# Performance work log

Measured on AMD Instinct MI355X. Metric: run time of the kernel, lower is better.

The kernel has to match this reference:

```python
import jax, jax.numpy as jnp
import numpy as np

L, H, D, DH, DFF = 6, 8, 512, 64, 2048
EPS = 1e-5


def setup_inputs() -> dict:
    key = jax.random.key(0)
    ks = jax.random.split(key, 20)
    B, S, T = 16, 512, 512
    s = 0.02
    inp = {
        "x": jax.random.normal(ks[0], (B, S, D), jnp.float32),
        "y": jax.random.normal(ks[1], (B, T, D), jnp.float32),
        # self-attention per-head projections, stacked over layers and heads
        "Wq1": jax.random.normal(ks[2], (L, H, D, DH), jnp.float32) * s,
        "Wk1": jax.random.normal(ks[3], (L, H, D, DH), jnp.float32) * s,
        "Wv1": jax.random.normal(ks[4], (L, H, D, DH), jnp.float32) * s,
        "Wo1": jax.random.normal(ks[5], (L, D, D), jnp.float32) * s,
        # cross-attention
        "Wq2": jax.random.normal(ks[6], (L, H, D, DH), jnp.float32) * s,
        "Wk2": jax.random.normal(ks[7], (L, H, D, DH), jnp.float32) * s,
        "Wv2": jax.random.normal(ks[8], (L, H, D, DH), jnp.float32) * s,
        "Wo2": jax.random.normal(ks[9], (L, D, D), jnp.float32) * s,
        # position-wise FFN
        "W1": jax.random.normal(ks[10], (L, D, DFF), jnp.float32) * s,
        "bf1": jnp.zeros((L, DFF), jnp.float32),
        "W2": jax.random.normal(ks[11], (L, DFF, D), jnp.float32) * s,
        "bf2": jnp.zeros((L, D), jnp.float32),
        # layer norms
        "ln1_g": jnp.ones((L, D), jnp.float32), "ln1_b": jnp.zeros((L, D), jnp.float32),
        "ln2_g": jnp.ones((L, D), jnp.float32), "ln2_b": jnp.zeros((L, D), jnp.float32),
        "ln3_g": jnp.ones((L, D), jnp.float32), "ln3_b": jnp.zeros((L, D), jnp.float32),
    }
    return inp


def _layer_norm(x, g, b):
    m = jnp.mean(x, axis=-1, keepdims=True)
    v = jnp.mean(jnp.square(x - m), axis=-1, keepdims=True)
    return (x - m) * jax.lax.rsqrt(v + EPS) * g + b


def _mha(q_in, kv_in, Wq, Wk, Wv, Wo, causal):
    # Wq/Wk/Wv: [H, D, DH]; batched equivalent of the per-head Linear loop
    q = jnp.einsum("bsd,hdk->bhsk", q_in, Wq)
    k = jnp.einsum("btd,hdk->bhtk", kv_in, Wk)
    v = jnp.einsum("btd,hdk->bhtk", kv_in, Wv)
    scores = jnp.einsum("bhsk,bhtk->bhst", q, k) / jnp.sqrt(jnp.float32(DH))
    if causal:
        S, T = scores.shape[-2], scores.shape[-1]
        mask = jnp.tril(jnp.ones((S, T), bool))
        scores = jnp.where(mask, scores, -jnp.inf)
    p = jax.nn.softmax(scores, axis=-1)
    out = jnp.einsum("bhst,bhtk->bhsk", p, v)
    B, _, S, _ = out.shape
    out = out.transpose(0, 2, 1, 3).reshape(B, S, H * DH)  # concat heads (dim=2 order)
    return out @ Wo


def reference(x, y, Wq1, Wk1, Wv1, Wo1, Wq2, Wk2, Wv2, Wo2,
              W1, bf1, W2, bf2, ln1_g, ln1_b, ln2_g, ln2_b, ln3_g, ln3_b):
    for l in range(L):
        # masked self-attention + residual + LN  (dropout = identity in eval)
        a1 = _mha(x, x, Wq1[l], Wk1[l], Wv1[l], Wo1[l], causal=True)
        h1 = _layer_norm(a1 + x, ln1_g[l], ln1_b[l])
        # cross-attention (queries from decoder, K/V from encoder output y)
        a2 = _mha(h1, y, Wq2[l], Wk2[l], Wv2[l], Wo2[l], causal=False)
        h2 = _layer_norm(a2 + h1, ln2_g[l], ln2_b[l])
        # position-wise FFN (batched over all positions)
        f = jax.nn.relu(h2 @ W1[l] + bf1[l]) @ W2[l] + bf2[l]
        x = _layer_norm(f + h2, ln3_g[l], ln3_b[l])
    return x
```

## Files before the change

kernel.cpp:

```cpp
#include <hip/hip_runtime.h>

typedef __bf16 bf16;
typedef __attribute__((ext_vector_type(8))) __bf16 bf16x8;
typedef __attribute__((ext_vector_type(4))) __bf16 bf16x4;
typedef __attribute__((ext_vector_type(4))) float f32x4;

#define GL16(gp, lp) __builtin_amdgcn_global_load_lds( \
    (const __attribute__((address_space(1))) unsigned int*)(gp), \
    (__attribute__((address_space(3))) unsigned int*)(lp), 16, 0, 0)

__device__ __forceinline__ f32x4 mfma16(bf16x8 a, bf16x8 b, f32x4 c) {
  return __builtin_amdgcn_mfma_f32_16x16x32_bf16(a, b, c, 0, 0, 0);
}

template<int BN, int RELU, int BIAS, int RES, int OUTB>
__global__ __launch_bounds__(256, 2) void gemm_k(
    const bf16* __restrict__ A, const bf16* __restrict__ Bt,
    float* __restrict__ Cf, bf16* __restrict__ Cb,
    const float* __restrict__ bias, const bf16* __restrict__ resid,
    int M, int N, int K)
{
  constexpr int MI = 4;
  constexpr int NI = BN / 32;
  __shared__ __align__(16) bf16 Al[3][128 * 32];
  __shared__ __align__(16) bf16 Bl[3][BN * 32];
  const int tid = threadIdx.x;
  const int wid = tid >> 6, lane = tid & 63;
  const int g = lane >> 4, l16 = lane & 15;

  int lin = blockIdx.x + gridDim.x * blockIdx.y;
  const int nwg = gridDim.x * gridDim.y;
  if ((nwg & 7) == 0) lin = (lin & 7) * (nwg >> 3) + (lin >> 3);
  const int bx = lin % gridDim.x, by = lin / gridDim.x;

  const int bm = by * 128, bn = bx * BN;
  const int wm = (wid >> 1) * 64;
  const int wn = (wid & 1) * (BN / 2);

  const f32x4 z4 = {0.f, 0.f, 0.f, 0.f};
  f32x4 acc[MI][NI];
#pragma unroll
  for (int i = 0; i < MI; ++i)
#pragma unroll
    for (int j = 0; j < NI; ++j) acc[i][j] = z4;

  const int srow = tid >> 2;
  const int scs = (((tid & 3) ^ ((srow >> 1) & 3)) * 8);
  const bf16* Ag = A + (size_t)(bm + srow) * K + scs;
  const bf16* Bg = Bt + (size_t)(bn + srow) * K + scs;
  const size_t half = (size_t)64 * K;

  auto stage = [&](int sel, int k0) {
    GL16(Ag + k0, &Al[sel][tid * 8]);
    GL16(Ag + k0 + half, &Al[sel][2048 + tid * 8]);
    GL16(Bg + k0, &Bl[sel][tid * 8]);
    if constexpr (BN == 128) GL16(Bg + k0 + half, &Bl[sel][2048 + tid * 8]);
  };
  constexpr int NL = 2 + BN / 64;

  const int nsteps = K >> 5;
  stage(0, 0);
  stage(1, 32);
  int cur = 0;
  for (int s = 0; s < nsteps; ++s) {
    __builtin_amdgcn_sched_barrier(0);
    if (s + 1 < nsteps) {
      if constexpr (NL == 4)
        asm volatile("s_waitcnt vmcnt(4)" ::: "memory");
      else
        asm volatile("s_waitcnt vmcnt(3)" ::: "memory");
    } else {
      asm volatile("s_waitcnt vmcnt(0)" ::: "memory");
    }
    __builtin_amdgcn_sched_barrier(0);
    __builtin_amdgcn_s_barrier();
    if (s + 2 < nsteps) {
      int pre = cur + 2; if (pre >= 3) pre -= 3;
      stage(pre, (s + 2) * 32);
    }
    bf16x8 af[MI], bfr[NI];
#pragma unroll
    for (int mi = 0; mi < MI; ++mi) {
      const int row = wm + mi * 16 + l16;
      af[mi] = *(const bf16x8*)&Al[cur][row * 32 + (g ^ ((row >> 1) & 3)) * 8];
    }
#pragma unroll
    for (int ni = 0; ni < NI; ++ni) {
      const int row = wn + ni * 16 + l16;
      bfr[ni] = *(const bf16x8*)&Bl[cur][row * 32 + (g ^ ((row >> 1) & 3)) * 8];
    }
#pragma unroll
    for (int mi = 0; mi < MI; ++mi)
#pragma unroll
      for (int ni = 0; ni < NI; ++ni)
        acc[mi][ni] = mfma16(af[mi], bfr[ni], acc[mi][ni]);
    ++cur; if (cur >= 3) cur = 0;
  }

#pragma unroll
  for (int mi = 0; mi < MI; ++mi) {
#pragma unroll
    for (int ni = 0; ni < NI; ++ni) {
#pragma unroll
      for (int r = 0; r < 4; ++r) {
        const int row = bm + wm + mi * 16 + g * 4 + r;
        const int col = bn + wn + ni * 16 + l16;
        float v = acc[mi][ni][r];
        if (BIAS) v += bias[col];
        const size_t idx = (size_t)row * N + col;
        if (RES)  v += (float)resid[idx];
        if (RELU) v = fmaxf(v, 0.f);
        if (OUTB) Cb[idx] = (bf16)v;
        else      Cf[idx] = v;
      }
    }
  }
}

template<int CAUSAL>
__global__ __launch_bounds__(256, 4) void attn_k(
    const bf16* __restrict__ Q, const bf16* __restrict__ Kg,
    const bf16* __restrict__ VT, bf16* __restrict__ O, int qs, int kvs)
{
  __shared__ __align__(16) bf16 Kl[2][64 * 64];
  __shared__ __align__(16) bf16 Vl[2][64 * 64];
  __shared__ __align__(16) bf16 plb[4 * 16 * 64];
  const int tid = threadIdx.x;
  const int wid = tid >> 6, lane = tid & 63;
  const int g = lane >> 4, l16 = lane & 15;

  int lin = blockIdx.x + 8 * blockIdx.y + 64 * blockIdx.z;
  lin = (lin & 7) * 128 + (lin >> 3);
  const int qt = lin & 7, h = (lin >> 3) & 7, b = lin >> 6;

  const int q0 = qt * 64 + wid * 16;
  const size_t tokQ = (size_t)b * 512 + q0;

  const bf16* qp = Q + (tokQ + l16) * (size_t)qs + h * 64 + g * 8;
  const bf16x8 qf0 = *(const bf16x8*)qp;
  const bf16x8 qf1 = *(const bf16x8*)(qp + 32);

  const int sr = tid >> 3;
  const int cs2 = ((((tid & 7) * 16) ^ ((sr & 7) << 4)) >> 1);
  const bf16* Ksrc = Kg + ((size_t)b * 512 + sr) * kvs + h * 64 + cs2;
  const bf16* Vsrc = VT + (size_t)(b * 8 + h) * 64 * 512 + (size_t)sr * 512 + cs2;
  bf16* pw = plb + wid * 1024;

  auto stage = [&](int sel, int t0) {
    GL16(Ksrc + (size_t)t0 * kvs, &Kl[sel][tid * 8]);
    GL16(Ksrc + (size_t)(t0 + 32) * kvs, &Kl[sel][tid * 8 + 2048]);
    GL16(Vsrc + t0, &Vl[sel][tid * 8]);
    GL16(Vsrc + 32 * 512 + t0, &Vl[sel][tid * 8 + 2048]);
  };

  const f32x4 z4 = {0.f, 0.f, 0.f, 0.f};
  float m[4], ls[4];
  f32x4 o[4];
#pragma unroll
  for (int r = 0; r < 4; ++r) { m[r] = -1e30f; ls[r] = 0.f; o[r] = z4; }

  const int sw = (l16 & 7) << 4;
  const int ktmax = CAUSAL ? qt : 7;
  stage(0, 0);
  int cur = 0;
  for (int kt = 0; kt <= ktmax; ++kt) {
    const int t0 = kt * 64;
    __builtin_amdgcn_sched_barrier(0);
    asm volatile("s_waitcnt vmcnt(0)" ::: "memory");
    __builtin_amdgcn_s_barrier();
    if (kt < ktmax) stage(cur ^ 1, t0 + 64);

    f32x4 sc[4];
#pragma unroll
    for (int jt = 0; jt < 4; ++jt) {
      const int rk = jt * 16 + l16;
      const bf16x8 kf0 = *(const bf16x8*)&Kl[cur][rk * 64 + (((g * 16) ^ sw) >> 1)];
      const bf16x8 kf1 = *(const bf16x8*)&Kl[cur][rk * 64 + (((g * 16 + 64) ^ sw) >> 1)];
      sc[jt] = mfma16(qf0, kf0, z4);
      sc[jt] = mfma16(qf1, kf1, sc[jt]);
    }
#pragma unroll
    for (int r = 0; r < 4; ++r) {
      const int q = g * 4 + r;
      const int srow = q0 + q;
      const int qs7 = (q & 7) << 4;
      float pv[4];
      float mx = -1e30f;
#pragma unroll
      for (int jt = 0; jt < 4; ++jt) {
        float v = sc[jt][r] * 0.125f;
        if (CAUSAL && (t0 + jt * 16 + l16) > srow) v = -1e30f;
        pv[jt] = v;
        mx = fmaxf(mx, v);
      }
#pragma unroll
      for (int msk = 8; msk; msk >>= 1) mx = fmaxf(mx, __shfl_xor(mx, msk));
      const float mn = fmaxf(m[r], mx);
      const float corr = __expf(m[r] - mn);
      float s = 0.f;
#pragma unroll
      for (int jt = 0; jt < 4; ++jt) {
        const float p = __expf(pv[jt] - mn);
        s += p;
        const int sb = (((jt * 16 + l16) * 2) ^ qs7) >> 1;
        pw[q * 64 + sb] = (bf16)p;
      }
#pragma unroll
      for (int msk = 8; msk; msk >>= 1) s += __shfl_xor(s, msk);
      ls[r] = ls[r] * corr + s;
      m[r] = mn;
#pragma unroll
      for (int j = 0; j < 4; ++j) o[j][r] *= corr;
    }
    asm volatile("s_waitcnt lgkmcnt(0)" ::: "memory");
    __builtin_amdgcn_sched_barrier(0);
    const bf16x8 pa0 = *(const bf16x8*)&pw[l16 * 64 + (((g * 16) ^ sw) >> 1)];
    const bf16x8 pa1 = *(const bf16x8*)&pw[l16 * 64 + (((g * 16 + 64) ^ sw) >> 1)];
#pragma unroll
    for (int j = 0; j < 4; ++j) {
      const int rv = j * 16 + l16;
      const bf16x8 vf0 = *(const bf16x8*)&Vl[cur][rv * 64 + (((g * 16) ^ sw) >> 1)];
      const bf16x8 vf1 = *(const bf16x8*)&Vl[cur][rv * 64 + (((g * 16 + 64) ^ sw) >> 1)];
      o[j] = mfma16(pa0, vf0, o[j]);
      o[j] = mfma16(pa1, vf1, o[j]);
    }
    cur ^= 1;
  }
#pragma unroll
  for (int r = 0; r < 4; ++r) {
    const float inv = 1.f / ls[r];
    bf16* op = O + (tokQ + g * 4 + r) * 512 + h * 64;
#pragma unroll
    for (int j = 0; j < 4; ++j) op[j * 16 + l16] = (bf16)(o[j][r] * inv);
  }
}

__global__ void vtrans(const bf16* __restrict__ src, bf16* __restrict__ dst,
                       int stride)
{
  __shared__ bf16 t[64][65];
  const int bh = blockIdx.z;
  const int b = bh >> 3, h = bh & 7;
  const int t0 = blockIdx.x * 64;
  const int tx = threadIdx.x, ty = threadIdx.y;
  src += ((size_t)b * 512 + t0) * stride + h * 64;
  dst += (size_t)bh * 64 * 512 + t0;
#pragma unroll
  for (int j = 0; j < 64; j += 4)
    t[ty + j][tx] = src[(size_t)(ty + j) * stride + tx];
  __syncthreads();
#pragma unroll
  for (int j = 0; j < 64; j += 4)
    dst[(size_t)(ty + j) * 512 + tx] = t[tx][ty + j];
}

__global__ __launch_bounds__(256) void ln_k(
    const float* __restrict__ z, const float* __restrict__ gam,
    const float* __restrict__ bet, float* __restrict__ of,
    bf16* __restrict__ ob)
{
  const int wid = threadIdx.x >> 6, lane = threadIdx.x & 63;
  const int row = blockIdx.x * 4 + wid;
  const f32x4* zr = (const f32x4*)(z + (size_t)row * 512);
  const f32x4 a = zr[lane], c = zr[lane + 64];
  float s = 0.f, ss = 0.f;
#pragma unroll
  for (int e = 0; e < 4; ++e) {
    s += a[e] + c[e];
    ss += a[e] * a[e] + c[e] * c[e];
  }
#pragma unroll
  for (int msk = 32; msk; msk >>= 1) {
    s += __shfl_xor(s, msk);
    ss += __shfl_xor(ss, msk);
  }
  const float mean = s * (1.f / 512.f);
  const float var = ss * (1.f / 512.f) - mean * mean;
  const float rstd = rsqrtf(var + 1e-5f);
  const f32x4* gp = (const f32x4*)gam;
  const f32x4* bp = (const f32x4*)bet;
  const f32x4 g0 = gp[lane], g1 = gp[lane + 64];
  const f32x4 b0 = bp[lane], b1 = bp[lane + 64];
  f32x4 o0, o1;
#pragma unroll
  for (int e = 0; e < 4; ++e) {
    o0[e] = (a[e] - mean) * rstd * g0[e] + b0[e];
    o1[e] = (c[e] - mean) * rstd * g1[e] + b1[e];
  }
  if (of) {
    f32x4* ofr = (f32x4*)(of + (size_t)row * 512);
    ofr[lane] = o0;
    ofr[lane + 64] = o1;
  }
  if (ob) {
    bf16x4 c0, c1;
#pragma unroll
    for (int e = 0; e < 4; ++e) { c0[e] = (bf16)o0[e]; c1[e] = (bf16)o1[e]; }
    bf16x4* obr = (bf16x4*)(ob + (size_t)row * 512);
    obr[lane] = c0;
    obr[lane + 64] = c1;
  }
}

__global__ void transpose_cast(const float* __restrict__ src, bf16* __restrict__ dst,
                               int R, int C, int bpl, size_t lstride, size_t boff)
{
  __shared__ float t[32][33];
  const int z = blockIdx.z;
  src += (size_t)z * R * C;
  dst += (size_t)(z / bpl) * lstride + (size_t)(z % bpl) * ((size_t)R * C) + boff;
  const int c0 = blockIdx.x * 32, r0 = blockIdx.y * 32;
  const int tx = threadIdx.x, ty = threadIdx.y;
#pragma unroll
  for (int j = 0; j < 32; j += 8)
    t[ty + j][tx] = src[(size_t)(r0 + ty + j) * C + c0 + tx];
  __syncthreads();
#pragma unroll
  for (int j = 0; j < 32; j += 8)
    dst[(size_t)(c0 + ty + j) * R + r0 + tx] = (bf16)t[tx][ty + j];
}

__global__ void cast4(const float* __restrict__ s, bf16* __restrict__ d)
{
  const int i = blockIdx.x * 256 + threadIdx.x;
  const f32x4 v = ((const f32x4*)s)[i];
  bf16x4 c;
#pragma unroll
  for (int e = 0; e < 4; ++e) c[e] = (bf16)v[e];
  ((bf16x4*)d)[i] = c;
}

extern "C" void kernel_launch(void* const* d_in, const int* in_sizes, int n_in,
                              void* d_out, int out_size, void* d_ws, size_t ws_size,
                              hipStream_t stream)
{
  (void)in_sizes; (void)n_in; (void)out_size; (void)ws_size;
  const float* x   = (const float*)d_in[0];
  const float* y   = (const float*)d_in[1];
  const float* Wq1 = (const float*)d_in[2];
  const float* Wk1 = (const float*)d_in[3];
  const float* Wv1 = (const float*)d_in[4];
  const float* Wo1 = (const float*)d_in[5];
  const float* Wq2 = (const float*)d_in[6];
  const float* Wk2 = (const float*)d_in[7];
  const float* Wv2 = (const float*)d_in[8];
  const float* Wo2 = (const float*)d_in[9];
  const float* W1  = (const float*)d_in[10];
  const float* b1  = (const float*)d_in[11];
  const float* W2  = (const float*)d_in[12];
  const float* b2  = (const float*)d_in[13];
  const float* ln1g = (const float*)d_in[14];
  const float* ln1b = (const float*)d_in[15];
  const float* ln2g = (const float*)d_in[16];
  const float* ln2b = (const float*)d_in[17];
  const float* ln3g = (const float*)d_in[18];
  const float* ln3b = (const float*)d_in[19];

  char* ws = (char*)d_ws;
  size_t off = 0;
  auto alloc = [&](size_t bytes) -> void* {
    void* p = (void*)(ws + off);
    off += (bytes + 255) & ~(size_t)255;
    return p;
  };

  bf16* wqkv1t = (bf16*)alloc((size_t)6 * 1536 * 512 * 2);
  bf16* wo1t   = (bf16*)alloc((size_t)6 * 512 * 512 * 2);
  bf16* wq2t   = (bf16*)alloc((size_t)6 * 512 * 512 * 2);
  bf16* wkv2t  = (bf16*)alloc((size_t)6 * 1024 * 512 * 2);
  bf16* wo2t   = (bf16*)alloc((size_t)6 * 512 * 512 * 2);
  bf16* w1t    = (bf16*)alloc((size_t)6 * 512 * 2048 * 2);
  bf16* w2t    = (bf16*)alloc((size_t)6 * 2048 * 512 * 2);
  bf16* xb   = (bf16*)alloc((size_t)8192 * 512 * 2);
  bf16* yb   = (bf16*)alloc((size_t)8192 * 512 * 2);
  bf16* qkvb = (bf16*)alloc((size_t)8192 * 1536 * 2);
  bf16* qb   = (bf16*)alloc((size_t)8192 * 512 * 2);
  bf16* kvb  = (bf16*)alloc((size_t)8192 * 1024 * 2);
  bf16* ab   = (bf16*)alloc((size_t)8192 * 512 * 2);
  bf16* h1b  = (bf16*)alloc((size_t)8192 * 512 * 2);
  bf16* h2b  = (bf16*)alloc((size_t)8192 * 512 * 2);
  float* zf  = (float*)alloc((size_t)8192 * 512 * 4);
  bf16* vt1  = (bf16*)alloc((size_t)8192 * 512 * 2);
  bf16* f1b  = qkvb;
  bf16* vt2  = qkvb;

  const dim3 tb(32, 8);
  transpose_cast<<<dim3(2, 16, 48), tb, 0, stream>>>(Wq1, wqkv1t, 512, 64, 8, (size_t)1536 * 512, 0);
  transpose_cast<<<dim3(2, 16, 48), tb, 0, stream>>>(Wk1, wqkv1t, 512, 64, 8, (size_t)1536 * 512, (size_t)512 * 512);
  transpose_cast<<<dim3(2, 16, 48), tb, 0, stream>>>(Wv1, wqkv1t, 512, 64, 8, (size_t)1536 * 512, (size_t)1024 * 512);
  transpose_cast<<<dim3(16, 16, 6), tb, 0, stream>>>(Wo1, wo1t, 512, 512, 1, (size_t)512 * 512, 0);
  transpose_cast<<<dim3(2, 16, 48), tb, 0, stream>>>(Wq2, wq2t, 512, 64, 8, (size_t)512 * 512, 0);
  transpose_cast<<<dim3(2, 16, 48), tb, 0, stream>>>(Wk2, wkv2t, 512, 64, 8, (size_t)1024 * 512, 0);
  transpose_cast<<<dim3(2, 16, 48), tb, 0, stream>>>(Wv2, wkv2t, 512, 64, 8, (size_t)1024 * 512, (size_t)512 * 512);
  transpose_cast<<<dim3(16, 16, 6), tb, 0, stream>>>(Wo2, wo2t, 512, 512, 1, (size_t)512 * 512, 0);
  transpose_cast<<<dim3(64, 16, 6), tb, 0, stream>>>(W1, w1t, 512, 2048, 1, (size_t)512 * 2048, 0);
  transpose_cast<<<dim3(16, 64, 6), tb, 0, stream>>>(W2, w2t, 2048, 512, 1, (size_t)2048 * 512, 0);
  cast4<<<4096, 256, 0, stream>>>(x, xb);
  cast4<<<4096, 256, 0, stream>>>(y, yb);

  const bf16* curxb = xb;
  const dim3 g512s(8, 64), g1024s(16, 64), g1536(12, 64), gff(16, 64);
  const dim3 vtg(8, 1, 128), vtb(64, 4);

  for (int l = 0; l < 6; ++l) {
    const bf16* WQKV1 = wqkv1t + (size_t)l * 1536 * 512;
    const bf16* WO1   = wo1t   + (size_t)l * 512 * 512;
    const bf16* WQ2   = wq2t   + (size_t)l * 512 * 512;
    const bf16* WKV2  = wkv2t  + (size_t)l * 1024 * 512;
    const bf16* WO2   = wo2t   + (size_t)l * 512 * 512;
    const bf16* W1T   = w1t    + (size_t)l * 2048 * 512;
    const bf16* W2T   = w2t    + (size_t)l * 512 * 2048;

    gemm_k<128, 0, 0, 0, 1><<<g1536, 256, 0, stream>>>(curxb, WQKV1, nullptr, qkvb,
                                                       nullptr, nullptr, 8192, 1536, 512);
    vtrans<<<vtg, vtb, 0, stream>>>(qkvb + 1024, vt1, 1536);
    attn_k<1><<<dim3(8, 8, 16), 256, 0, stream>>>(qkvb, qkvb + 512, vt1, ab, 1536, 1536);
    gemm_k<64, 0, 0, 1, 0><<<g512s, 256, 0, stream>>>(ab, WO1, zf, nullptr,
                                                      nullptr, curxb, 8192, 512, 512);
    ln_k<<<2048, 256, 0, stream>>>(zf, ln1g + l * 512, ln1b + l * 512, nullptr, h1b);

    gemm_k<64, 0, 0, 0, 1><<<g512s, 256, 0, stream>>>(h1b, WQ2, nullptr, qb,
                                                      nullptr, nullptr, 8192, 512, 512);
    gemm_k<64, 0, 0, 0, 1><<<g1024s, 256, 0, stream>>>(yb, WKV2, nullptr, kvb,
                                                       nullptr, nullptr, 8192, 1024, 512);
    vtrans<<<vtg, vtb, 0, stream>>>(kvb + 512, vt2, 1024);
    attn_k<0><<<dim3(8, 8, 16), 256, 0, stream>>>(qb, kvb, vt2, ab, 512, 1024);
    gemm_k<64, 0, 0, 1, 0><<<g512s, 256, 0, stream>>>(ab, WO2, zf, nullptr,
                                                      nullptr, h1b, 8192, 512, 512);
    ln_k<<<2048, 256, 0, stream>>>(zf, ln2g + l * 512, ln2b + l * 512, nullptr, h2b);

    gemm_k<128, 1, 1, 0, 1><<<gff, 256, 0, stream>>>(h2b, W1T, nullptr, f1b,
                                                     b1 + l * 2048, nullptr, 8192, 2048, 512);
    gemm_k<64, 0, 1, 1, 0><<<g512s, 256, 0, stream>>>(f1b, W2T, zf, nullptr,
                                                      b2 + l * 512, h2b, 8192, 512, 2048);
    float* outf = (l == 5) ? (float*)d_out : nullptr;
    bf16* outb  = (l == 5) ? nullptr : xb;
    ln_k<<<2048, 256, 0, stream>>>(zf, ln3g + l * 512, ln3b + l * 512, outf, outb);
    curxb = xb;
  }
}
```

Measured before the change: 1.417 ms.

## Fuse V transpose into projection GEMM epilogue and switch GEMM to BK=64 double-buffering

The QKV and KV projection GEMMs now write the V columns straight into the transposed per-head layout that attention reads, so the two separate vtrans launches per layer are removed. The GEMM main loop also moves from a 3-stage, 32-wide K pipeline to a 2-stage, 64-wide K tile with a new XOR swizzle. The 64-wide variant gets a higher occupancy hint in its launch bounds. In exchange, the kernel waits on all outstanding loads every step, which exposes more load latency, and the transposed V stores are strided 8-byte writes.

```diff
diff --git a/kernel.cpp b/kernel.cpp
--- a/kernel.cpp
+++ b/kernel.cpp
@@ -13,17 +13,18 @@
   return __builtin_amdgcn_mfma_f32_16x16x32_bf16(a, b, c, 0, 0, 0);
 }
 
-template<int BN, int RELU, int BIAS, int RES, int OUTB>
-__global__ __launch_bounds__(256, 2) void gemm_k(
+template<int BN, int RELU, int BIAS, int RES, int OUTB, int VTO>
+__global__ __launch_bounds__(256, (BN == 64) ? 3 : 2) void gemm_k(
     const bf16* __restrict__ A, const bf16* __restrict__ Bt,
     float* __restrict__ Cf, bf16* __restrict__ Cb,
     const float* __restrict__ bias, const bf16* __restrict__ resid,
+    bf16* __restrict__ vt, int vtc0,
     int M, int N, int K)
 {
   constexpr int MI = 4;
   constexpr int NI = BN / 32;
-  __shared__ __align__(16) bf16 Al[3][128 * 32];
-  __shared__ __align__(16) bf16 Bl[3][BN * 32];
+  __shared__ __align__(16) bf16 Al[2][128 * 64];
+  __shared__ __align__(16) bf16 Bl[2][BN * 64];
   const int tid = threadIdx.x;
   const int wid = tid >> 6, lane = tid & 63;
   const int g = lane >> 4, l16 = lane & 15;
@@ -44,57 +45,73 @@
 #pragma unroll
     for (int j = 0; j < NI; ++j) acc[i][j] = z4;
 
-  const int srow = tid >> 2;
-  const int scs = (((tid & 3) ^ ((srow >> 1) & 3)) * 8);
-  const bf16* Ag = A + (size_t)(bm + srow) * K + scs;
-  const bf16* Bg = Bt + (size_t)(bn + srow) * K + scs;
-  const size_t half = (size_t)64 * K;
+  const int sr = tid >> 3;
+  const int scs = ((((tid & 7) * 16) ^ ((sr & 7) << 4)) >> 1);
+  const bf16* Ag = A + (size_t)(bm + sr) * K + scs;
+  const bf16* Bg = Bt + (size_t)(bn + sr) * K + scs;
+  const size_t kstep32 = (size_t)32 * K;
 
   auto stage = [&](int sel, int k0) {
-    GL16(Ag + k0, &Al[sel][tid * 8]);
-    GL16(Ag + k0 + half, &Al[sel][2048 + tid * 8]);
-    GL16(Bg + k0, &Bl[sel][tid * 8]);
-    if constexpr (BN == 128) GL16(Bg + k0 + half, &Bl[sel][2048 + tid * 8]);
+#pragma unroll
+    for (int sw = 0; sw < 4; ++sw)
+      GL16(Ag + k0 + sw * kstep32, &Al[sel][sw * 2048 + tid * 8]);
+#pragma unroll
+    for (int sw = 0; sw < BN / 32; ++sw)
+      GL16(Bg + k0 + sw * kstep32, &Bl[sel][sw * 2048 + tid * 8]);
   };
-  constexpr int NL = 2 + BN / 64;
-
-  const int nsteps = K >> 5;
+
+  const int nsteps = K >> 6;
   stage(0, 0);
-  stage(1, 32);
   int cur = 0;
   for (int s = 0; s < nsteps; ++s) {
     __builtin_amdgcn_sched_barrier(0);
-    if (s + 1 < nsteps) {
-      if constexpr (NL == 4)
-        asm volatile("s_waitcnt vmcnt(4)" ::: "memory");
-      else
-        asm volatile("s_waitcnt vmcnt(3)" ::: "memory");
-    } else {
-      asm volatile("s_waitcnt vmcnt(0)" ::: "memory");
-    }
+    asm volatile("s_waitcnt vmcnt(0)" ::: "memory");
+    __builtin_amdgcn_s_barrier();
     __builtin_amdgcn_sched_barrier(0);
-    __builtin_amdgcn_s_barrier();
-    if (s + 2 < nsteps) {
-      int pre = cur + 2; if (pre >= 3) pre -= 3;
-      stage(pre, (s + 2) * 32);
-    }
-    bf16x8 af[MI], bfr[NI];
+    if (s + 1 < nsteps) stage(cur ^ 1, (s + 1) * 64);
+    bf16x8 af[MI][2], bfr[NI][2];
 #pragma unroll
     for (int mi = 0; mi < MI; ++mi) {
       const int row = wm + mi * 16 + l16;
-      af[mi] = *(const bf16x8*)&Al[cur][row * 32 + (g ^ ((row >> 1) & 3)) * 8];
+      const int rs = (row & 7) << 4;
+#pragma unroll
+      for (int kh = 0; kh < 2; ++kh)
+        af[mi][kh] = *(const bf16x8*)&Al[cur][row * 64 + (((g * 16 + kh * 64) ^ rs) >> 1)];
     }
 #pragma unroll
     for (int ni = 0; ni < NI; ++ni) {
       const int row = wn + ni * 16 + l16;
-      bfr[ni] = *(const bf16x8*)&Bl[cur][row * 32 + (g ^ ((row >> 1) & 3)) * 8];
-    }
-#pragma unroll
-    for (int mi = 0; mi < MI; ++mi)
-#pragma unroll
-      for (int ni = 0; ni < NI; ++ni)
-        acc[mi][ni] = mfma16(af[mi], bfr[ni], acc[mi][ni]);
-    ++cur; if (cur >= 3) cur = 0;
+      const int rs = (row & 7) << 4;
+#pragma unroll
+      for (int kh = 0; kh < 2; ++kh)
+        bfr[ni][kh] = *(const bf16x8*)&Bl[cur][row * 64 + (((g * 16 + kh * 64) ^ rs) >> 1)];
+    }
+#pragma unroll
+    for (int kh = 0; kh < 2; ++kh)
+#pragma unroll
+      for (int mi = 0; mi < MI; ++mi)
+#pragma unroll
+        for (int ni = 0; ni < NI; ++ni)
+          acc[mi][ni] = mfma16(af[mi][kh], bfr[ni][kh], acc[mi][ni]);
+    cur ^= 1;
+  }
+
+  if (VTO && bn >= vtc0) {
+#pragma unroll
+    for (int mi = 0; mi < MI; ++mi) {
+#pragma unroll
+      for (int ni = 0; ni < NI; ++ni) {
+        const int row0 = bm + wm + mi * 16 + g * 4;
+        const int gdh = bn + wn + ni * 16 + l16 - vtc0;
+        const int bh = (row0 >> 9) * 8 + (gdh >> 6);
+        const int t0 = row0 & 511;
+        bf16x4 v4;
+#pragma unroll
+        for (int r = 0; r < 4; ++r) v4[r] = (bf16)acc[mi][ni][r];
+        *(bf16x4*)&vt[((size_t)bh * 64 + (gdh & 63)) * 512 + t0] = v4;
+      }
+    }
+    return;
   }
 
 #pragma unroll
@@ -233,25 +250,6 @@
 #pragma unroll
     for (int j = 0; j < 4; ++j) op[j * 16 + l16] = (bf16)(o[j][r] * inv);
   }
-}
-
-__global__ void vtrans(const bf16* __restrict__ src, bf16* __restrict__ dst,
-                       int stride)
-{
-  __shared__ bf16 t[64][65];
-  const int bh = blockIdx.z;
-  const int b = bh >> 3, h = bh & 7;
-  const int t0 = blockIdx.x * 64;
-  const int tx = threadIdx.x, ty = threadIdx.y;
-  src += ((size_t)b * 512 + t0) * stride + h * 64;
-  dst += (size_t)bh * 64 * 512 + t0;
-#pragma unroll
-  for (int j = 0; j < 64; j += 4)
-    t[ty + j][tx] = src[(size_t)(ty + j) * stride + tx];
-  __syncthreads();
-#pragma unroll
-  for (int j = 0; j < 64; j += 4)
-    dst[(size_t)(ty + j) * 512 + tx] = t[tx][ty + j];
 }
 
 __global__ __launch_bounds__(256) void ln_k(
@@ -400,7 +398,6 @@
 
   const bf16* curxb = xb;
   const dim3 g512s(8, 64), g1024s(16, 64), g1536(12, 64), gff(16, 64);
-  const dim3 vtg(8, 1, 128), vtb(64, 4);
 
   for (int l = 0; l < 6; ++l) {
     const bf16* WQKV1 = wqkv1t + (size_t)l * 1536 * 512;
@@ -411,28 +408,26 @@
     const bf16* W1T   = w1t    + (size_t)l * 2048 * 512;
     const bf16* W2T   = w2t    + (size_t)l * 512 * 2048;
 
-    gemm_k<128, 0, 0, 0, 1><<<g1536, 256, 0, stream>>>(curxb, WQKV1, nullptr, qkvb,
-                                                       nullptr, nullptr, 8192, 1536, 512);
-    vtrans<<<vtg, vtb, 0, stream>>>(qkvb + 1024, vt1, 1536);
+    gemm_k<128, 0, 0, 0, 1, 1><<<g1536, 256, 0, stream>>>(curxb, WQKV1, nullptr, qkvb,
+                                                          nullptr, nullptr, vt1, 1024, 8192, 1536, 512);
     attn_k<1><<<dim3(8, 8, 16), 256, 0, stream>>>(qkvb, qkvb + 512, vt1, ab, 1536, 1536);
-    gemm_k<64, 0, 0, 1, 0><<<g512s, 256, 0, stream>>>(ab, WO1, zf, nullptr,
-                                                      nullptr, curxb, 8192, 512, 512);
+    gemm_k<64, 0, 0, 1, 0, 0><<<g512s, 256, 0, stream>>>(ab, WO1, zf, nullptr,
+                                                         nullptr, curxb, nullptr, 0, 8192, 512, 512);
     ln_k<<<2048, 256, 0, stream>>>(zf, ln1g + l * 512, ln1b + l * 512, nullptr, h1b);
 
-    gemm_k<64, 0, 0, 0, 1><<<g512s, 256, 0, stream>>>(h1b, WQ2, nullptr, qb,
-                                                      nullptr, nullptr, 8192, 512, 512);
-    gemm_k<64, 0, 0, 0, 1><<<g1024s, 256, 0, stream>>>(yb, WKV2, nullptr, kvb,
-                                                       nullptr, nullptr, 8192, 1024, 512);
-    vtrans<<<vtg, vtb, 0, stream>>>(kvb + 512, vt2, 1024);
+    gemm_k<64, 0, 0, 0, 1, 0><<<g512s, 256, 0, stream>>>(h1b, WQ2, nullptr, qb,
+                                                         nullptr, nullptr, nullptr, 0, 8192, 512, 512);
+    gemm_k<64, 0, 0, 0, 1, 1><<<g1024s, 256, 0, stream>>>(yb, WKV2, nullptr, kvb,
+                                                          nullptr, nullptr, vt2, 512, 8192, 1024, 512);
     attn_k<0><<<dim3(8, 8, 16), 256, 0, stream>>>(qb, kvb, vt2, ab, 512, 1024);
-    gemm_k<64, 0, 0, 1, 0><<<g512s, 256, 0, stream>>>(ab, WO2, zf, nullptr,
-                                                      nullptr, h1b, 8192, 512, 512);
+    gemm_k<64, 0, 0, 1, 0, 0><<<g512s, 256, 0, stream>>>(ab, WO2, zf, nullptr,
+                                                         nullptr, h1b, nullptr, 0, 8192, 512, 512);
     ln_k<<<2048, 256, 0, stream>>>(zf, ln2g + l * 512, ln2b + l * 512, nullptr, h2b);
 
-    gemm_k<128, 1, 1, 0, 1><<<gff, 256, 0, stream>>>(h2b, W1T, nullptr, f1b,
-                                                     b1 + l * 2048, nullptr, 8192, 2048, 512);
-    gemm_k<64, 0, 1, 1, 0><<<g512s, 256, 0, stream>>>(f1b, W2T, zf, nullptr,
-                                                      b2 + l * 512, h2b, 8192, 512, 2048);
+    gemm_k<128, 1, 1, 0, 1, 0><<<gff, 256, 0, stream>>>(h2b, W1T, nullptr, f1b,
+                                                        b1 + l * 2048, nullptr, nullptr, 0, 8192, 2048, 512);
+    gemm_k<64, 0, 1, 1, 0, 0><<<g512s, 256, 0, stream>>>(f1b, W2T, zf, nullptr,
+                                                         b2 + l * 512, h2b, nullptr, 0, 8192, 512, 2048);
     float* outf = (l == 5) ? (float*)d_out : nullptr;
     bf16* outb  = (l == 5) ? nullptr : xb;
     ln_k<<<2048, 256, 0, stream>>>(zf, ln3g + l * 512, ln3b + l * 512, outf, outb);
```

Result: faster. 1.288 ms (-9.1%).
